# Performance work log

Measured on AMD Instinct MI355X. Metric: run time of the kernel, lower is better.

Reference implementation:

```python
import jax, jax.numpy as jnp
import numpy as np

T, D, H, E, A = 4096, 1024, 2048, 8, 2


def setup_inputs() -> dict:
    key = jax.random.key(0)
    k1, k2, k3, k4, k5 = jax.random.split(key, 5)
    x = jax.random.normal(k1, (T, D), dtype=jnp.float32)
    expert_indices = jax.random.randint(k2, (T, A), 0, E, dtype=jnp.int64)
    scale = 0.02  # keep activations numerically sane (torch.randn init is unscaled)
    w_gate = jax.random.normal(k3, (E, H, D), dtype=jnp.float32) * scale
    w_up = jax.random.normal(k4, (E, H, D), dtype=jnp.float32) * scale
    w_down = jax.random.normal(k5, (E, D, H), dtype=jnp.float32) * scale
    return {"x": x, "expert_indices": expert_indices,
            "w_gate": w_gate, "w_up": w_up, "w_down": w_down}


def reference(x, expert_indices, w_gate, w_up, w_down):
    # Math identical to: gather per-token expert weights then einsum, but
    # computed as dense all-expert GEMMs + small activation gathers so we
    # never materialize the (T, A, H, D) gathered weight tensors.
    zg = jnp.einsum('td,ehd->teh', x, w_gate)   # (T, E, H)
    zu = jnp.einsum('td,ehd->teh', x, w_up)     # (T, E, H)
    idx = expert_indices[:, :, None]            # (T, A, 1)
    g = jnp.take_along_axis(zg, idx, axis=1)    # (T, A, H)
    u = jnp.take_along_axis(zu, idx, axis=1)    # (T, A, H)
    h = jax.nn.silu(g) * u                      # (T, A, H)
    # Down projection: route h back to its expert with one-hot, dense GEMM.
    oh = jax.nn.one_hot(expert_indices, E, dtype=h.dtype)  # (T, A, E)
    he = jnp.einsum('tah,tae->taeh', h, oh)     # (T, A, E, H)
    out = jnp.einsum('taeh,edh->tad', he, w_down)  # (T, A, D)
    return out
```

## Files before the change

kernel.cpp:

```cpp
#include <hip/hip_runtime.h>

#define NE 8
#define TA 8192
#define MAXT 40
#define MAXPAD (MAXT*256)

typedef __attribute__((ext_vector_type(4)))  float f32x4;
typedef __attribute__((ext_vector_type(16))) float f32x16;
typedef __attribute__((ext_vector_type(8)))  short s16x8;

#define WS_CUR  8
#define WS_META 16
#define WS_TEXP 18
#define WS_PERM 256

#define WAITVM(N) asm volatile("s_waitcnt vmcnt(" #N ")" ::: "memory")
#define BAR()     asm volatile("s_barrier" ::: "memory")

__device__ __forceinline__ unsigned short f2bf(float f) {
  unsigned u = __builtin_bit_cast(unsigned, f);
  u += 0x7FFFu + ((u >> 16) & 1u);
  return (unsigned short)(u >> 16);
}

__device__ __forceinline__ void glds16(const unsigned short* g, unsigned short* l) {
  __builtin_amdgcn_global_load_lds(
      (const __attribute__((address_space(1))) unsigned int*)g,
      (__attribute__((address_space(3))) unsigned int*)l, 16, 0, 0);
}

__global__ void k_route(const int* __restrict__ idx, int* __restrict__ ws) {
  __shared__ int cnt[NE];
  int t = threadIdx.x;
  if (t < NE) cnt[t] = 0;
  __syncthreads();
  int e0[8];
#pragma unroll
  for (int k = 0; k < 8; ++k) { e0[k] = idx[t + k * 1024]; atomicAdd(&cnt[e0[k]], 1); }
  __syncthreads();
  if (t == 0) {
    int off = 0, ti = 0;
    for (int e = 0; e < NE; ++e) {
      ws[WS_CUR + e] = off;
      int c = cnt[e];
      int ntl = (c + 255) >> 8;
      for (int k = 0; k < ntl; ++k) ws[WS_TEXP + ti++] = e;
      off += ntl << 8;
    }
    ws[WS_META] = ti;
    ws[WS_META + 1] = off;
  }
#pragma unroll
  for (int k = 0; k < MAXPAD / 1024; ++k) ws[WS_PERM + t + k * 1024] = -1;
  __syncthreads();
#pragma unroll
  for (int k = 0; k < 8; ++k) {
    int p = atomicAdd(&ws[WS_CUR + e0[k]], 1);
    ws[WS_PERM + p] = t + k * 1024;
  }
}

__global__ void k_cvt_gu2(const float* __restrict__ g, const float* __restrict__ u,
                          unsigned short* __restrict__ d) {
  int t = blockIdx.x * 256 + threadIdx.x;
  int i = t * 8;
  int dd = i & 1023;
  int h = (i >> 10) & 2047;
  int e = i >> 21;
  int dr = (e << 12) + ((h >> 5) << 6) + (h & 31);
  f32x4 a = *(const f32x4*)(g + i);
  f32x4 b = *(const f32x4*)(g + i + 4);
  s16x8 o;
  o[0] = (short)f2bf(a[0]); o[1] = (short)f2bf(a[1]);
  o[2] = (short)f2bf(a[2]); o[3] = (short)f2bf(a[3]);
  o[4] = (short)f2bf(b[0]); o[5] = (short)f2bf(b[1]);
  o[6] = (short)f2bf(b[2]); o[7] = (short)f2bf(b[3]);
  *(s16x8*)(d + (size_t)dr * 1024 + dd) = o;
  a = *(const f32x4*)(u + i);
  b = *(const f32x4*)(u + i + 4);
  o[0] = (short)f2bf(a[0]); o[1] = (short)f2bf(a[1]);
  o[2] = (short)f2bf(a[2]); o[3] = (short)f2bf(a[3]);
  o[4] = (short)f2bf(b[0]); o[5] = (short)f2bf(b[1]);
  o[6] = (short)f2bf(b[2]); o[7] = (short)f2bf(b[3]);
  *(s16x8*)(d + (size_t)(dr + 32) * 1024 + dd) = o;
}

__global__ void k_cvt(const float* __restrict__ s, unsigned short* __restrict__ d) {
  int i = (blockIdx.x * 256 + threadIdx.x) * 8;
  f32x4 a = *(const f32x4*)(s + i);
  f32x4 b = *(const f32x4*)(s + i + 4);
  s16x8 o;
  o[0] = (short)f2bf(a[0]); o[1] = (short)f2bf(a[1]);
  o[2] = (short)f2bf(a[2]); o[3] = (short)f2bf(a[3]);
  o[4] = (short)f2bf(b[0]); o[5] = (short)f2bf(b[1]);
  o[6] = (short)f2bf(b[2]); o[7] = (short)f2bf(b[3]);
  *(s16x8*)(d + i) = o;
}

__global__ void k_gather(const float* __restrict__ x, const int* __restrict__ ws,
                         unsigned short* __restrict__ xb) {
  int tid = blockIdx.x * 256 + threadIdx.x;
  int r = tid >> 7;
  int c = (tid & 127) << 3;
  int ta = ws[WS_PERM + r];
  s16x8 o = {0,0,0,0,0,0,0,0};
  if (ta >= 0) {
    const float* xp = x + (size_t)(ta >> 1) * 1024 + c;
    f32x4 a = *(const f32x4*)xp;
    f32x4 b = *(const f32x4*)(xp + 4);
    o[0] = (short)f2bf(a[0]); o[1] = (short)f2bf(a[1]);
    o[2] = (short)f2bf(a[2]); o[3] = (short)f2bf(a[3]);
    o[4] = (short)f2bf(b[0]); o[5] = (short)f2bf(b[1]);
    o[6] = (short)f2bf(b[2]); o[7] = (short)f2bf(b[3]);
  }
  *(s16x8*)(xb + (size_t)r * 1024 + c) = o;
}


#define STG(LB, H, K0, RSTEP)                                          \
  {                                                                    \
    unsigned short* Ld = (LB) + (H) * 8192 + tid * 8;                  \
    int ko = (K0) + (H) * 32;                                          \
    glds16(gAs + ko,           Ld);                                    \
    glds16(gAs + ko + (RSTEP), Ld + 4096);                             \
    glds16(gBs + ko,           Ld + 16384);                            \
    glds16(gBs + ko + (RSTEP), Ld + 16384 + 4096);                     \
  }

__global__ __launch_bounds__(512) void k_gemm1(
    const unsigned short* __restrict__ xb, const unsigned short* __restrict__ wgu,
    unsigned short* __restrict__ hb, const int* __restrict__ ws) {
  int mt = blockIdx.y;
  if (mt >= ws[WS_META]) return;
  int e = ws[WS_TEXP + mt];
  int nt = blockIdx.x;

  __shared__ unsigned short L[2][32768];

  int tid = threadIdx.x;
  int lane = tid & 63, wid = tid >> 6;
  int wm = wid >> 2, wn = wid & 3;
  int r31 = lane & 31, kg = lane >> 5, x3 = r31 & 3;

  int rl  = tid >> 2;
  int csw = (tid & 3) ^ (rl & 3);

  const unsigned short* gAs = xb  + (size_t)(mt * 256 + rl) * 1024 + csw * 8;
  const unsigned short* gBs = wgu + (size_t)(e * 4096 + nt * 256 + rl) * 1024 + csw * 8;

  f32x16 accg[4] = {};
  f32x16 accu[4] = {};

  int aof0 = (wm * 128 + r31) * 32;
  int aof1 = aof0 + 1024;
  int aof2 = aof0 + 2048;
  int aof3 = aof0 + 3072;
  int bgo  = (wn * 64 + r31) * 32;

#define CMP1(LC, P)                                                          \
  {                                                                          \
    const unsigned short* Ab = (LC) + (P) * 8192;                            \
    const unsigned short* Bb = Ab + 16384;                                   \
    _Pragma("unroll")                                                        \
    for (int ksl = 0; ksl < 2; ++ksl) {                                      \
      int sc = ((kg + 2 * ksl) ^ x3) << 3;                                   \
      s16x8 a0 = *(const s16x8*)&Ab[aof0 + sc];                              \
      s16x8 a1 = *(const s16x8*)&Ab[aof1 + sc];                              \
      s16x8 a2 = *(const s16x8*)&Ab[aof2 + sc];                              \
      s16x8 a3 = *(const s16x8*)&Ab[aof3 + sc];                              \
      s16x8 bg = *(const s16x8*)&Bb[bgo + sc];                               \
      s16x8 bu = *(const s16x8*)&Bb[bgo + 1024 + sc];                        \
      __builtin_amdgcn_s_setprio(1);                                         \
      accg[0] = __builtin_amdgcn_mfma_f32_32x32x16_bf16(a0, bg, accg[0], 0,0,0); \
      accu[0] = __builtin_amdgcn_mfma_f32_32x32x16_bf16(a0, bu, accu[0], 0,0,0); \
      accg[1] = __builtin_amdgcn_mfma_f32_32x32x16_bf16(a1, bg, accg[1], 0,0,0); \
      accu[1] = __builtin_amdgcn_mfma_f32_32x32x16_bf16(a1, bu, accu[1], 0,0,0); \
      accg[2] = __builtin_amdgcn_mfma_f32_32x32x16_bf16(a2, bg, accg[2], 0,0,0); \
      accu[2] = __builtin_amdgcn_mfma_f32_32x32x16_bf16(a2, bu, accu[2], 0,0,0); \
      accg[3] = __builtin_amdgcn_mfma_f32_32x32x16_bf16(a3, bg, accg[3], 0,0,0); \
      accu[3] = __builtin_amdgcn_mfma_f32_32x32x16_bf16(a3, bu, accu[3], 0,0,0); \
      __builtin_amdgcn_s_setprio(0);                                         \
    }                                                                        \
  }

  STG(&L[0][0], 0, 0, 131072)
  STG(&L[0][0], 1, 0, 131072)

#pragma unroll 2
  for (int kt = 0; kt < 16; ++kt) {
    unsigned short* Lc = &L[kt & 1][0];
    unsigned short* Ln = &L[(kt & 1) ^ 1][0];
    int kn = (kt + 1 < 16 ? kt + 1 : kt) * 64;
    WAITVM(4); BAR();
    STG(Ln, 0, kn, 131072)
    CMP1(Lc, 0)
    WAITVM(4); BAR();
    STG(Ln, 1, kn, 131072)
    CMP1(Lc, 1)
  }
  WAITVM(0);

  int hrow0 = mt * 256 + wm * 128;
  int hcol  = nt * 128 + wn * 32 + r31;
#pragma unroll
  for (int mi = 0; mi < 4; ++mi)
#pragma unroll
    for (int r = 0; r < 16; ++r) {
      int crow = (r & 3) + 8 * (r >> 2) + 4 * kg;
      float g = accg[mi][r];
      float u = accu[mi][r];
      float h = (g / (1.f + __expf(-g))) * u;
      hb[(size_t)(hrow0 + mi * 32 + crow) * 2048 + hcol] = f2bf(h);
    }
}

__global__ __launch_bounds__(512) void k_gemm2(
    const unsigned short* __restrict__ hb, const unsigned short* __restrict__ wdb,
    float* __restrict__ out, const int* __restrict__ ws) {
  int mt = blockIdx.y;
  if (mt >= ws[WS_META]) return;
  int e = ws[WS_TEXP + mt];
  int nt = blockIdx.x & 3;
  int kslice = blockIdx.x >> 2;
  int kb = kslice * 1024;

  __shared__ unsigned short L[2][32768];

  int tid = threadIdx.x;
  int lane = tid & 63, wid = tid >> 6;
  int wm = wid >> 2, wn = wid & 3;
  int r31 = lane & 31, kg = lane >> 5, x3 = r31 & 3;

  int rl  = tid >> 2;
  int csw = (tid & 3) ^ (rl & 3);

  const unsigned short* gAs = hb  + (size_t)(mt * 256 + rl) * 2048 + kb + csw * 8;
  const unsigned short* gBs = wdb + (size_t)(e * 1024 + nt * 256 + rl) * 2048 + kb + csw * 8;

  f32x16 acc0[4] = {};
  f32x16 acc1[4] = {};

  int aof0 = (wm * 128 + r31) * 32;
  int aof1 = aof0 + 1024;
  int aof2 = aof0 + 2048;
  int aof3 = aof0 + 3072;
  int bgo  = (wn * 64 + r31) * 32;

#define CMP2(LC, P)                                                          \
  {                                                                          \
    const unsigned short* Ab = (LC) + (P) * 8192;                            \
    const unsigned short* Bb = Ab + 16384;                                   \
    _Pragma("unroll")                                                        \
    for (int ksl = 0; ksl < 2; ++ksl) {                                      \
      int sc = ((kg + 2 * ksl) ^ x3) << 3;                                   \
      s16x8 a0 = *(const s16x8*)&Ab[aof0 + sc];                              \
      s16x8 a1 = *(const s16x8*)&Ab[aof1 + sc];                              \
      s16x8 a2 = *(const s16x8*)&Ab[aof2 + sc];                              \
      s16x8 a3 = *(const s16x8*)&Ab[aof3 + sc];                              \
      s16x8 b0 = *(const s16x8*)&Bb[bgo + sc];                               \
      s16x8 b1 = *(const s16x8*)&Bb[bgo + 1024 + sc];                        \
      __builtin_amdgcn_s_setprio(1);                                         \
      acc0[0] = __builtin_amdgcn_mfma_f32_32x32x16_bf16(a0, b0, acc0[0], 0,0,0); \
      acc1[0] = __builtin_amdgcn_mfma_f32_32x32x16_bf16(a0, b1, acc1[0], 0,0,0); \
      acc0[1] = __builtin_amdgcn_mfma_f32_32x32x16_bf16(a1, b0, acc0[1], 0,0,0); \
      acc1[1] = __builtin_amdgcn_mfma_f32_32x32x16_bf16(a1, b1, acc1[1], 0,0,0); \
      acc0[2] = __builtin_amdgcn_mfma_f32_32x32x16_bf16(a2, b0, acc0[2], 0,0,0); \
      acc1[2] = __builtin_amdgcn_mfma_f32_32x32x16_bf16(a2, b1, acc1[2], 0,0,0); \
      acc0[3] = __builtin_amdgcn_mfma_f32_32x32x16_bf16(a3, b0, acc0[3], 0,0,0); \
      acc1[3] = __builtin_amdgcn_mfma_f32_32x32x16_bf16(a3, b1, acc1[3], 0,0,0); \
      __builtin_amdgcn_s_setprio(0);                                         \
    }                                                                        \
  }

  STG(&L[0][0], 0, 0, 262144)
  STG(&L[0][0], 1, 0, 262144)

#pragma unroll 2
  for (int kt = 0; kt < 16; ++kt) {
    unsigned short* Lc = &L[kt & 1][0];
    unsigned short* Ln = &L[(kt & 1) ^ 1][0];
    int kn = (kt + 1 < 16 ? kt + 1 : kt) * 64;
    WAITVM(4); BAR();
    STG(Ln, 0, kn, 262144)
    CMP2(Lc, 0)
    WAITVM(4); BAR();
    STG(Ln, 1, kn, 262144)
    CMP2(Lc, 1)
  }
  WAITVM(0);

  int prow0 = mt * 256 + wm * 128;
  int dcol  = nt * 256 + wn * 64 + r31;
#pragma unroll
  for (int mi = 0; mi < 4; ++mi)
#pragma unroll
    for (int r = 0; r < 16; ++r) {
      int crow = (r & 3) + 8 * (r >> 2) + 4 * kg;
      int ta = ws[WS_PERM + prow0 + mi * 32 + crow];
      if (ta >= 0) {
        unsafeAtomicAdd(&out[(size_t)ta * 1024 + dcol],      acc0[mi][r]);
        unsafeAtomicAdd(&out[(size_t)ta * 1024 + dcol + 32], acc1[mi][r]);
      }
    }
}

extern "C" void kernel_launch(void* const* d_in, const int* in_sizes, int n_in,
                              void* d_out, int out_size, void* d_ws, size_t ws_size,
                              hipStream_t stream) {
  const float* x   = (const float*)d_in[0];
  const int*   idx = (const int*)d_in[1];
  const float* wg  = (const float*)d_in[2];
  const float* wu  = (const float*)d_in[3];
  const float* wd  = (const float*)d_in[4];
  float* out = (float*)d_out;

  int*  wsi = (int*)d_ws;
  char* wsb = (char*)d_ws;
  const size_t OFF_XB  = 65536;
  const size_t OFF_WDB = 65536;
  const size_t OFF_WGU = 65536 + (size_t)NE * 1024 * 2048 * 2;
  const size_t OFF_HB  = OFF_WGU + (size_t)NE * 4096 * 1024 * 2;
  unsigned short* xbuf = (unsigned short*)(wsb + OFF_XB);
  unsigned short* wdb  = (unsigned short*)(wsb + OFF_WDB);
  unsigned short* wgu  = (unsigned short*)(wsb + OFF_WGU);
  unsigned short* hb   = (unsigned short*)(wsb + OFF_HB);

  k_route<<<1, 1024, 0, stream>>>(idx, wsi);
  k_cvt_gu2<<<(NE * 2048 * 1024) / (256 * 8), 256, 0, stream>>>(wg, wu, wgu);
  k_gather<<<(MAXPAD * 128) / 256, 256, 0, stream>>>(x, wsi, xbuf);

  k_gemm1<<<dim3(16, MAXT), 512, 0, stream>>>(xbuf, wgu, hb, wsi);

  k_cvt<<<(NE * 1024 * 2048) / (256 * 8), 256, 0, stream>>>(wd, wdb);

  hipMemsetAsync(out, 0, (size_t)out_size * sizeof(float), stream);
  k_gemm2<<<dim3(8, MAXT), 512, 0, stream>>>(hb, wdb, out, wsi);
}
```

Measured before the change: 330.3 us.

## Shrink GEMM tiles to 128x128, drop split-K atomics and output memset

```diff
diff --git a/kernel.cpp b/kernel.cpp
--- a/kernel.cpp
+++ b/kernel.cpp
@@ -15,6 +15,7 @@
 #define WS_PERM 256
 
 #define WAITVM(N) asm volatile("s_waitcnt vmcnt(" #N ")" ::: "memory")
+#define LGKM0()   asm volatile("s_waitcnt lgkmcnt(0)" ::: "memory")
 #define BAR()     asm volatile("s_barrier" ::: "memory")
 
 __device__ __forceinline__ unsigned short f2bf(float f) {
@@ -117,191 +118,126 @@
 }
 
 
-#define STG(LB, H, K0, RSTEP)                                          \
+#define STG(BUF, KSH, KO)                                              \
   {                                                                    \
-    unsigned short* Ld = (LB) + (H) * 8192 + tid * 8;                  \
-    int ko = (K0) + (H) * 32;                                          \
-    glds16(gAs + ko,           Ld);                                    \
-    glds16(gAs + ko + (RSTEP), Ld + 4096);                             \
-    glds16(gBs + ko,           Ld + 16384);                            \
-    glds16(gBs + ko + (RSTEP), Ld + 16384 + 4096);                     \
-  }
-
-__global__ __launch_bounds__(512) void k_gemm1(
+    unsigned short* ld = &L[BUF][(KSH) * 4096 + tid * 8];              \
+    glds16(gA + (KO), ld);                                             \
+    glds16(gB + (KO), ld + 8192);                                      \
+  }
+
+#define PHASE(BUF, KSH, KON, ACC0, ACC1)                               \
+  {                                                                    \
+    WAITVM(2);                                                         \
+    BAR();                                                             \
+    STG((BUF) ^ 1, KSH, KON);                                          \
+    const unsigned short* Lb = &L[BUF][(KSH) * 4096];                  \
+    s16x8 a0 = *(const s16x8*)&Lb[aoff + sca0];                        \
+    s16x8 a1 = *(const s16x8*)&Lb[aoff + sca1];                        \
+    s16x8 b00 = *(const s16x8*)&Lb[boff + scb0];                       \
+    s16x8 b01 = *(const s16x8*)&Lb[boff + 1024 + scb0];                \
+    s16x8 b10 = *(const s16x8*)&Lb[boff + scb1];                       \
+    s16x8 b11 = *(const s16x8*)&Lb[boff + 1024 + scb1];                \
+    __builtin_amdgcn_s_setprio(1);                                     \
+    ACC0 = __builtin_amdgcn_mfma_f32_32x32x16_bf16(a0, b00, ACC0, 0, 0, 0); \
+    ACC1 = __builtin_amdgcn_mfma_f32_32x32x16_bf16(a0, b01, ACC1, 0, 0, 0); \
+    ACC0 = __builtin_amdgcn_mfma_f32_32x32x16_bf16(a1, b10, ACC0, 0, 0, 0); \
+    ACC1 = __builtin_amdgcn_mfma_f32_32x32x16_bf16(a1, b11, ACC1, 0, 0, 0); \
+    __builtin_amdgcn_s_setprio(0);                                     \
+    LGKM0();                                                           \
+    BAR();                                                             \
+  }
+
+#define GEOM_COMMON                                                    \
+  int tid = threadIdx.x, lane = tid & 63, wid = tid >> 6;              \
+  int wm = wid >> 1, wn = wid & 1;                                     \
+  int r31 = lane & 31, kg = lane >> 5;                                 \
+  int sr = tid >> 2, sp = tid & 3;                                     \
+  int ss = sp ^ ((sr >> 1) & 3);                                       \
+  int ra = wm * 32 + r31;                                              \
+  int rb = wn * 64 + r31;                                              \
+  int swa = (ra >> 1) & 3, swb = (rb >> 1) & 3;                        \
+  int aoff = ra * 32;                                                  \
+  int boff = 8192 + rb * 32;                                           \
+  int sca0 = ((kg ^ swa)) << 3, sca1 = (((2 | kg) ^ swa)) << 3;        \
+  int scb0 = ((kg ^ swb)) << 3, scb1 = (((2 | kg) ^ swb)) << 3;
+
+__global__ __launch_bounds__(512, 4) void k_gemm1(
     const unsigned short* __restrict__ xb, const unsigned short* __restrict__ wgu,
     unsigned short* __restrict__ hb, const int* __restrict__ ws) {
   int mt = blockIdx.y;
-  if (mt >= ws[WS_META]) return;
-  int e = ws[WS_TEXP + mt];
+  if (mt >= ws[WS_META] * 2) return;
+  int e = ws[WS_TEXP + (mt >> 1)];
   int nt = blockIdx.x;
 
-  __shared__ unsigned short L[2][32768];
-
-  int tid = threadIdx.x;
-  int lane = tid & 63, wid = tid >> 6;
-  int wm = wid >> 2, wn = wid & 3;
-  int r31 = lane & 31, kg = lane >> 5, x3 = r31 & 3;
-
-  int rl  = tid >> 2;
-  int csw = (tid & 3) ^ (rl & 3);
-
-  const unsigned short* gAs = xb  + (size_t)(mt * 256 + rl) * 1024 + csw * 8;
-  const unsigned short* gBs = wgu + (size_t)(e * 4096 + nt * 256 + rl) * 1024 + csw * 8;
-
-  f32x16 accg[4] = {};
-  f32x16 accu[4] = {};
-
-  int aof0 = (wm * 128 + r31) * 32;
-  int aof1 = aof0 + 1024;
-  int aof2 = aof0 + 2048;
-  int aof3 = aof0 + 3072;
-  int bgo  = (wn * 64 + r31) * 32;
-
-#define CMP1(LC, P)                                                          \
-  {                                                                          \
-    const unsigned short* Ab = (LC) + (P) * 8192;                            \
-    const unsigned short* Bb = Ab + 16384;                                   \
-    _Pragma("unroll")                                                        \
-    for (int ksl = 0; ksl < 2; ++ksl) {                                      \
-      int sc = ((kg + 2 * ksl) ^ x3) << 3;                                   \
-      s16x8 a0 = *(const s16x8*)&Ab[aof0 + sc];                              \
-      s16x8 a1 = *(const s16x8*)&Ab[aof1 + sc];                              \
-      s16x8 a2 = *(const s16x8*)&Ab[aof2 + sc];                              \
-      s16x8 a3 = *(const s16x8*)&Ab[aof3 + sc];                              \
-      s16x8 bg = *(const s16x8*)&Bb[bgo + sc];                               \
-      s16x8 bu = *(const s16x8*)&Bb[bgo + 1024 + sc];                        \
-      __builtin_amdgcn_s_setprio(1);                                         \
-      accg[0] = __builtin_amdgcn_mfma_f32_32x32x16_bf16(a0, bg, accg[0], 0,0,0); \
-      accu[0] = __builtin_amdgcn_mfma_f32_32x32x16_bf16(a0, bu, accu[0], 0,0,0); \
-      accg[1] = __builtin_amdgcn_mfma_f32_32x32x16_bf16(a1, bg, accg[1], 0,0,0); \
-      accu[1] = __builtin_amdgcn_mfma_f32_32x32x16_bf16(a1, bu, accu[1], 0,0,0); \
-      accg[2] = __builtin_amdgcn_mfma_f32_32x32x16_bf16(a2, bg, accg[2], 0,0,0); \
-      accu[2] = __builtin_amdgcn_mfma_f32_32x32x16_bf16(a2, bu, accu[2], 0,0,0); \
-      accg[3] = __builtin_amdgcn_mfma_f32_32x32x16_bf16(a3, bg, accg[3], 0,0,0); \
-      accu[3] = __builtin_amdgcn_mfma_f32_32x32x16_bf16(a3, bu, accu[3], 0,0,0); \
-      __builtin_amdgcn_s_setprio(0);                                         \
-    }                                                                        \
-  }
-
-  STG(&L[0][0], 0, 0, 131072)
-  STG(&L[0][0], 1, 0, 131072)
+  __shared__ unsigned short L[2][16384];
+
+  GEOM_COMMON
+
+  const unsigned short* gA = xb  + (size_t)(mt * 128 + sr) * 1024 + ss * 8;
+  const unsigned short* gB = wgu + (size_t)(e * 4096 + nt * 128 + sr) * 1024 + ss * 8;
+
+  f32x16 accg = {}, accu = {};
+
+  STG(0, 0, 0)
+  STG(0, 1, 32)
 
 #pragma unroll 2
-  for (int kt = 0; kt < 16; ++kt) {
-    unsigned short* Lc = &L[kt & 1][0];
-    unsigned short* Ln = &L[(kt & 1) ^ 1][0];
-    int kn = (kt + 1 < 16 ? kt + 1 : kt) * 64;
-    WAITVM(4); BAR();
-    STG(Ln, 0, kn, 131072)
-    CMP1(Lc, 0)
-    WAITVM(4); BAR();
-    STG(Ln, 1, kn, 131072)
-    CMP1(Lc, 1)
-  }
-  WAITVM(0);
-
-  int hrow0 = mt * 256 + wm * 128;
-  int hcol  = nt * 128 + wn * 32 + r31;
-#pragma unroll
-  for (int mi = 0; mi < 4; ++mi)
-#pragma unroll
-    for (int r = 0; r < 16; ++r) {
-      int crow = (r & 3) + 8 * (r >> 2) + 4 * kg;
-      float g = accg[mi][r];
-      float u = accu[mi][r];
-      float h = (g / (1.f + __expf(-g))) * u;
-      hb[(size_t)(hrow0 + mi * 32 + crow) * 2048 + hcol] = f2bf(h);
-    }
-}
-
-__global__ __launch_bounds__(512) void k_gemm2(
+  for (int t = 0; t < 16; ++t) {
+    int tn = (t + 1 < 16 ? t + 1 : t) * 64;
+    PHASE(t & 1, 0, tn,      accg, accu)
+    PHASE(t & 1, 1, tn + 32, accg, accu)
+  }
+
+  int hrow0 = mt * 128 + wm * 32;
+  int hcol  = (nt * 2 + wn) * 32 + r31;
+#pragma unroll
+  for (int r = 0; r < 16; ++r) {
+    int crow = (r & 3) + 8 * (r >> 2) + 4 * kg;
+    float g = accg[r];
+    float u = accu[r];
+    float h = (g / (1.f + __expf(-g))) * u;
+    hb[(size_t)(hrow0 + crow) * 2048 + hcol] = f2bf(h);
+  }
+}
+
+__global__ __launch_bounds__(512, 4) void k_gemm2(
     const unsigned short* __restrict__ hb, const unsigned short* __restrict__ wdb,
     float* __restrict__ out, const int* __restrict__ ws) {
   int mt = blockIdx.y;
-  if (mt >= ws[WS_META]) return;
-  int e = ws[WS_TEXP + mt];
-  int nt = blockIdx.x & 3;
-  int kslice = blockIdx.x >> 2;
-  int kb = kslice * 1024;
-
-  __shared__ unsigned short L[2][32768];
-
-  int tid = threadIdx.x;
-  int lane = tid & 63, wid = tid >> 6;
-  int wm = wid >> 2, wn = wid & 3;
-  int r31 = lane & 31, kg = lane >> 5, x3 = r31 & 3;
-
-  int rl  = tid >> 2;
-  int csw = (tid & 3) ^ (rl & 3);
-
-  const unsigned short* gAs = hb  + (size_t)(mt * 256 + rl) * 2048 + kb + csw * 8;
-  const unsigned short* gBs = wdb + (size_t)(e * 1024 + nt * 256 + rl) * 2048 + kb + csw * 8;
-
-  f32x16 acc0[4] = {};
-  f32x16 acc1[4] = {};
-
-  int aof0 = (wm * 128 + r31) * 32;
-  int aof1 = aof0 + 1024;
-  int aof2 = aof0 + 2048;
-  int aof3 = aof0 + 3072;
-  int bgo  = (wn * 64 + r31) * 32;
-
-#define CMP2(LC, P)                                                          \
-  {                                                                          \
-    const unsigned short* Ab = (LC) + (P) * 8192;                            \
-    const unsigned short* Bb = Ab + 16384;                                   \
-    _Pragma("unroll")                                                        \
-    for (int ksl = 0; ksl < 2; ++ksl) {                                      \
-      int sc = ((kg + 2 * ksl) ^ x3) << 3;                                   \
-      s16x8 a0 = *(const s16x8*)&Ab[aof0 + sc];                              \
-      s16x8 a1 = *(const s16x8*)&Ab[aof1 + sc];                              \
-      s16x8 a2 = *(const s16x8*)&Ab[aof2 + sc];                              \
-      s16x8 a3 = *(const s16x8*)&Ab[aof3 + sc];                              \
-      s16x8 b0 = *(const s16x8*)&Bb[bgo + sc];                               \
-      s16x8 b1 = *(const s16x8*)&Bb[bgo + 1024 + sc];                        \
-      __builtin_amdgcn_s_setprio(1);                                         \
-      acc0[0] = __builtin_amdgcn_mfma_f32_32x32x16_bf16(a0, b0, acc0[0], 0,0,0); \
-      acc1[0] = __builtin_amdgcn_mfma_f32_32x32x16_bf16(a0, b1, acc1[0], 0,0,0); \
-      acc0[1] = __builtin_amdgcn_mfma_f32_32x32x16_bf16(a1, b0, acc0[1], 0,0,0); \
-      acc1[1] = __builtin_amdgcn_mfma_f32_32x32x16_bf16(a1, b1, acc1[1], 0,0,0); \
-      acc0[2] = __builtin_amdgcn_mfma_f32_32x32x16_bf16(a2, b0, acc0[2], 0,0,0); \
-      acc1[2] = __builtin_amdgcn_mfma_f32_32x32x16_bf16(a2, b1, acc1[2], 0,0,0); \
-      acc0[3] = __builtin_amdgcn_mfma_f32_32x32x16_bf16(a3, b0, acc0[3], 0,0,0); \
-      acc1[3] = __builtin_amdgcn_mfma_f32_32x32x16_bf16(a3, b1, acc1[3], 0,0,0); \
-      __builtin_amdgcn_s_setprio(0);                                         \
-    }                                                                        \
-  }
-
-  STG(&L[0][0], 0, 0, 262144)
-  STG(&L[0][0], 1, 0, 262144)
+  if (mt >= ws[WS_META] * 2) return;
+  int e = ws[WS_TEXP + (mt >> 1)];
+  int nt = blockIdx.x;
+
+  __shared__ unsigned short L[2][16384];
+
+  GEOM_COMMON
+
+  const unsigned short* gA = hb  + (size_t)(mt * 128 + sr) * 2048 + ss * 8;
+  const unsigned short* gB = wdb + (size_t)(e * 1024 + nt * 128 + sr) * 2048 + ss * 8;
+
+  f32x16 acc0 = {}, acc1 = {};
+
+  STG(0, 0, 0)
+  STG(0, 1, 32)
 
 #pragma unroll 2
-  for (int kt = 0; kt < 16; ++kt) {
-    unsigned short* Lc = &L[kt & 1][0];
-    unsigned short* Ln = &L[(kt & 1) ^ 1][0];
-    int kn = (kt + 1 < 16 ? kt + 1 : kt) * 64;
-    WAITVM(4); BAR();
-    STG(Ln, 0, kn, 262144)
-    CMP2(Lc, 0)
-    WAITVM(4); BAR();
-    STG(Ln, 1, kn, 262144)
-    CMP2(Lc, 1)
-  }
-  WAITVM(0);
-
-  int prow0 = mt * 256 + wm * 128;
-  int dcol  = nt * 256 + wn * 64 + r31;
-#pragma unroll
-  for (int mi = 0; mi < 4; ++mi)
-#pragma unroll
-    for (int r = 0; r < 16; ++r) {
-      int crow = (r & 3) + 8 * (r >> 2) + 4 * kg;
-      int ta = ws[WS_PERM + prow0 + mi * 32 + crow];
-      if (ta >= 0) {
-        unsafeAtomicAdd(&out[(size_t)ta * 1024 + dcol],      acc0[mi][r]);
-        unsafeAtomicAdd(&out[(size_t)ta * 1024 + dcol + 32], acc1[mi][r]);
-      }
+  for (int t = 0; t < 32; ++t) {
+    int tn = (t + 1 < 32 ? t + 1 : t) * 64;
+    PHASE(t & 1, 0, tn,      acc0, acc1)
+    PHASE(t & 1, 1, tn + 32, acc0, acc1)
+  }
+
+  int prow0 = mt * 128 + wm * 32;
+  int dcol  = nt * 128 + wn * 64 + r31;
+#pragma unroll
+  for (int r = 0; r < 16; ++r) {
+    int crow = (r & 3) + 8 * (r >> 2) + 4 * kg;
+    int ta = ws[WS_PERM + prow0 + crow];
+    if (ta >= 0) {
+      out[(size_t)ta * 1024 + dcol]      = acc0[r];
+      out[(size_t)ta * 1024 + dcol + 32] = acc1[r];
     }
+  }
 }
 
 extern "C" void kernel_launch(void* const* d_in, const int* in_sizes, int n_in,
@@ -329,10 +265,9 @@
   k_cvt_gu2<<<(NE * 2048 * 1024) / (256 * 8), 256, 0, stream>>>(wg, wu, wgu);
   k_gather<<<(MAXPAD * 128) / 256, 256, 0, stream>>>(x, wsi, xbuf);
 
-  k_gemm1<<<dim3(16, MAXT), 512, 0, stream>>>(xbuf, wgu, hb, wsi);
+  k_gemm1<<<dim3(32, MAXT * 2), 512, 0, stream>>>(xbuf, wgu, hb, wsi);
 
   k_cvt<<<(NE * 1024 * 2048) / (256 * 8), 256, 0, stream>>>(wd, wdb);
 
-  hipMemsetAsync(out, 0, (size_t)out_size * sizeof(float), stream);
-  k_gemm2<<<dim3(8, MAXT), 512, 0, stream>>>(hb, wdb, out, wsi);
-}
+  k_gemm2<<<dim3(8, MAXT * 2), 512, 0, stream>>>(hb, wdb, out, wsi);
+}
```

Measured after the change: 266.4 us. -19.4%, faster.
